# Performance work log

Hardware: AMD Instinct MI355X
Metric: run time of the kernel (lower is better)

Reference implementation:

```python
import jax, jax.numpy as jnp
import numpy as np

DIM = 512
HEADS = 8
HEAD_DIM = DIM // HEADS
SCALE = HEAD_DIM ** -0.5
CPB_HIDDEN = 512
N_CLASSES = 2
LN_EPS = 1e-5


def _layernorm(x, g, b):
    m = jnp.mean(x, axis=-1, keepdims=True)
    v = jnp.var(x, axis=-1, keepdims=True)
    return (x - m) / jnp.sqrt(v + LN_EPS) * g + b


def _coord_attention(x, coords, cpb_w1, cpb_b1, cpb_w2, cpb_b2, qkv_w, qkv_b, proj_w, proj_b):
    B, N, C = x.shape
    qkv = (x @ qkv_w + qkv_b).reshape(B, N, 3, HEADS, HEAD_DIM)
    q, k, v = jnp.moveaxis(qkv, 2, 0)  # each (B, N, H, hd)
    attn = jnp.einsum('bnhd,bmhd->bhnm', q * SCALE, k)  # (B, H, N, N)
    rel = coords[:, :, None, :] - coords[:, None, :, :]  # (B, N, N, 2)
    rel = rel / (jnp.linalg.norm(rel, axis=-1, keepdims=True) + 1e-6)
    bias = jax.nn.relu(rel @ cpb_w1 + cpb_b1) @ cpb_w2 + cpb_b2  # (B, N, N, H)
    attn = jax.nn.softmax(attn + jnp.transpose(bias, (0, 3, 1, 2)), axis=-1)
    out = jnp.einsum('bhnm,bmhd->bnhd', attn, v).reshape(B, N, C)
    return out @ proj_w + proj_b


def setup_inputs() -> dict:
    key = jax.random.key(0)
    ks = iter(jax.random.split(key, 32))
    d = {}
    d['h'] = jax.random.normal(next(ks), (1, 400, 1024), dtype=jnp.float32)
    d['coords'] = jax.random.uniform(next(ks), (1, 400, 2), dtype=jnp.float32) * 1000.0
    def lin(kw, kb, fan_in, fan_out):
        w = jax.random.normal(kw, (fan_in, fan_out), dtype=jnp.float32) / np.sqrt(fan_in)
        b = jax.random.normal(kb, (fan_out,), dtype=jnp.float32) * 0.01
        return w, b
    d['fc1_w'], d['fc1_b'] = lin(next(ks), next(ks), 1024, DIM)
    d['cls_token'] = jax.random.normal(next(ks), (1, 1, DIM), dtype=jnp.float32)
    for p in ('l1', 'l2'):
        d[p + '_norm_g'] = jnp.ones((DIM,), jnp.float32)
        d[p + '_norm_b'] = jnp.zeros((DIM,), jnp.float32)
        d[p + '_cpb_w1'], d[p + '_cpb_b1'] = lin(next(ks), next(ks), 2, CPB_HIDDEN)
        d[p + '_cpb_w2'], d[p + '_cpb_b2'] = lin(next(ks), next(ks), CPB_HIDDEN, HEADS)
        d[p + '_qkv_w'], d[p + '_qkv_b'] = lin(next(ks), next(ks), DIM, 3 * DIM)
        d[p + '_proj_w'], d[p + '_proj_b'] = lin(next(ks), next(ks), DIM, DIM)
    d['norm_g'] = jnp.ones((DIM,), jnp.float32)
    d['norm_b'] = jnp.zeros((DIM,), jnp.float32)
    d['fc2_w'], d['fc2_b'] = lin(next(ks), next(ks), DIM, N_CLASSES)
    return d


def reference(h, coords, fc1_w, fc1_b, cls_token,
              l1_norm_g, l1_norm_b, l1_cpb_w1, l1_cpb_b1, l1_cpb_w2, l1_cpb_b2,
              l1_qkv_w, l1_qkv_b, l1_proj_w, l1_proj_b,
              l2_norm_g, l2_norm_b, l2_cpb_w1, l2_cpb_b1, l2_cpb_w2, l2_cpb_b2,
              l2_qkv_w, l2_qkv_b, l2_proj_w, l2_proj_b,
              norm_g, norm_b, fc2_w, fc2_b):
    B, Np, _ = h.shape
    h = jax.nn.relu(h @ fc1_w + fc1_b)  # (B, N, 512)
    side = int(np.ceil(np.sqrt(Np)))
    add = side * side - Np  # pad bag to a perfect square (wrap-around copy)
    h = jnp.concatenate([h, h[:, :add, :]], axis=1)
    coords = jnp.concatenate([coords, coords[:, :add, :]], axis=1)
    cls = jnp.broadcast_to(cls_token, (B, 1, DIM))
    h = jnp.concatenate([cls, h], axis=1)
    coords = jnp.concatenate([jnp.zeros((B, 1, 2), h.dtype), coords], axis=1)
    h = h + _coord_attention(_layernorm(h, l1_norm_g, l1_norm_b), coords,
                             l1_cpb_w1, l1_cpb_b1, l1_cpb_w2, l1_cpb_b2,
                             l1_qkv_w, l1_qkv_b, l1_proj_w, l1_proj_b)
    h = h + _coord_attention(_layernorm(h, l2_norm_g, l2_norm_b), coords,
                             l2_cpb_w1, l2_cpb_b1, l2_cpb_w2, l2_cpb_b2,
                             l2_qkv_w, l2_qkv_b, l2_proj_w, l2_proj_b)
    h = _layernorm(h, norm_g, norm_b)[:, 0]  # CLS token
    return h @ fc2_w + fc2_b  # (B, n_classes)
```

## Files before the change

### kernel.cpp

```cpp
#include <hip/hip_runtime.h>
#include <math.h>

#define NP 401
#define DIM 512
#define LN_EPS 1e-5f
#define ATT_SCALE 0.125f
#define CPB_M 4096
#define TSTRIDE (CPB_M + 64)
#define PVS (401L * 512)

template<bool TB, typename LA, typename LB>
__device__ __forceinline__ void gemm64(
    int kBeg, int kEnd, int tid,
    float (*as)[68], float (*bs)[68], float (&acc)[4][4],
    LA&& loadA, LB&& loadB)
{
    float aR[4], bR[4];
    loadA(kBeg, aR);
    loadB(kBeg, bR);
    for (int k0 = kBeg; k0 < kEnd; k0 += 16) {
        const int arow = tid >> 2, aq = tid & 3;
        as[aq * 4 + 0][arow] = aR[0];
        as[aq * 4 + 1][arow] = aR[1];
        as[aq * 4 + 2][arow] = aR[2];
        as[aq * 4 + 3][arow] = aR[3];
        if (!TB) {
            *(float4*)&bs[tid >> 4][(tid & 15) * 4] =
                make_float4(bR[0], bR[1], bR[2], bR[3]);
        } else {
            bs[aq * 4 + 0][arow] = bR[0];
            bs[aq * 4 + 1][arow] = bR[1];
            bs[aq * 4 + 2][arow] = bR[2];
            bs[aq * 4 + 3][arow] = bR[3];
        }
        __syncthreads();
        float nA[4] = {0.f,0.f,0.f,0.f}, nB[4] = {0.f,0.f,0.f,0.f};
        if (k0 + 16 < kEnd) { loadA(k0 + 16, nA); loadB(k0 + 16, nB); }
        const int tx = tid & 15, ty = tid >> 4;
        #pragma unroll
        for (int kk = 0; kk < 16; ++kk) {
            float4 a4 = *(const float4*)&as[kk][ty * 4];
            float4 b4 = *(const float4*)&bs[kk][tx * 4];
            float av[4] = {a4.x, a4.y, a4.z, a4.w};
            float bv[4] = {b4.x, b4.y, b4.z, b4.w};
            #pragma unroll
            for (int r = 0; r < 4; ++r)
                #pragma unroll
                for (int c = 0; c < 4; ++c)
                    acc[r][c] = fmaf(av[r], bv[c], acc[r][c]);
        }
        __syncthreads();
        #pragma unroll
        for (int j = 0; j < 4; ++j) { aR[j] = nA[j]; bR[j] = nB[j]; }
    }
}

__global__ __launch_bounds__(256) void gemm_bias_kernel(
    const float* __restrict__ A,
    const float* __restrict__ B, int ldb,
    const float* __restrict__ bias,
    float* __restrict__ C, int ldc)
{
    __shared__ float as[16][68], bs[16][68];
    const int tid = threadIdx.x;
    const int m0 = blockIdx.x * 64, n0 = blockIdx.y * 64;
    float acc[4][4] = {};

    auto loadA = [&](int k0, float r[4]) {
        int gm = m0 + (tid >> 2);
        if (gm > 400) { r[0]=r[1]=r[2]=r[3]=0.f; return; }
        int gk = k0 + (tid & 3) * 4;
        float4 v = *(const float4*)(A + (long)gm * 512 + gk);
        r[0]=v.x; r[1]=v.y; r[2]=v.z; r[3]=v.w;
    };
    auto loadB = [&](int k0, float r[4]) {
        int gk = k0 + (tid >> 4);
        int gn = n0 + (tid & 15) * 4;
        float4 v = *(const float4*)(B + (long)gk * ldb + gn);
        r[0]=v.x; r[1]=v.y; r[2]=v.z; r[3]=v.w;
    };
    gemm64<false>(0, 512, tid, as, bs, acc, loadA, loadB);

    const int tx = tid & 15, ty = tid >> 4;
    const float4 bv = *(const float4*)(bias + n0 + tx * 4);
    #pragma unroll
    for (int r = 0; r < 4; ++r) {
        int m = m0 + ty * 4 + r;
        if (m > 400) continue;
        *(float4*)&C[(long)m * ldc + n0 + tx * 4] =
            make_float4(acc[r][0] + bv.x, acc[r][1] + bv.y,
                        acc[r][2] + bv.z, acc[r][3] + bv.w);
    }
}

__global__ __launch_bounds__(256) void flash_kernel(
    const float* __restrict__ qkv,
    const int* __restrict__ pm, const float* __restrict__ pf,
    const float* __restrict__ T,
    float* __restrict__ PO,
    float* __restrict__ Pml)
{
    __shared__ float as[16][68], bs[16][68];
    __shared__ float pT[64][68];
    __shared__ float vs[64][68];
    const int tid = threadIdx.x;
    const int m0 = blockIdx.x * 64, nb = blockIdx.y, h = blockIdx.z;
    const int n0 = nb * 64;
    float acc[4][4] = {};

    float vreg[4][4];
    {
        int key = n0 + (tid >> 2);
        int d0 = (tid & 3) * 16;
        if (key <= 400) {
            const float* p = qkv + (long)key * 1536 + 1024 + h * 64 + d0;
            #pragma unroll
            for (int i = 0; i < 4; ++i) {
                float4 v = *(const float4*)(p + i * 4);
                vreg[i][0] = v.x; vreg[i][1] = v.y;
                vreg[i][2] = v.z; vreg[i][3] = v.w;
            }
        } else {
            #pragma unroll
            for (int i = 0; i < 4; ++i)
                vreg[i][0] = vreg[i][1] = vreg[i][2] = vreg[i][3] = 0.f;
        }
    }

    auto loadQ = [&](int k0, float r[4]) {
        int gm = m0 + (tid >> 2);
        if (gm > 400) { r[0]=r[1]=r[2]=r[3]=0.f; return; }
        int gk = k0 + (tid & 3) * 4;
        float4 v = *(const float4*)(qkv + (long)gm * 1536 + h * 64 + gk);
        r[0]=v.x; r[1]=v.y; r[2]=v.z; r[3]=v.w;
    };
    auto loadK = [&](int k0, float r[4]) {
        int gn = n0 + (tid >> 2);
        if (gn > 400) { r[0]=r[1]=r[2]=r[3]=0.f; return; }
        int gk = k0 + (tid & 3) * 4;
        float4 v = *(const float4*)(qkv + (long)gn * 1536 + 512 + h * 64 + gk);
        r[0]=v.x; r[1]=v.y; r[2]=v.z; r[3]=v.w;
    };
    gemm64<true>(0, 64, tid, as, bs, acc, loadQ, loadK);

    {
        int key = tid >> 2, d0 = (tid & 3) * 16;
        #pragma unroll
        for (int i = 0; i < 4; ++i)
            *(float4*)&vs[key][d0 + i * 4] =
                make_float4(vreg[i][0], vreg[i][1], vreg[i][2], vreg[i][3]);
    }

    const int tx = tid & 15, ty = tid >> 4;
    const float* Tt = T + (long)h * TSTRIDE;
    float p[4][4];
    #pragma unroll
    for (int r = 0; r < 4; ++r) {
        int i = m0 + ty * 4 + r;
        float sv[4];
        #pragma unroll
        for (int c = 0; c < 4; ++c) {
            int j = n0 + tx * 4 + c;
            if (i <= 400 && j <= 400) {
                int id = i * 416 + j;
                int mm = pm[id];
                float fr = pf[id];
                float t0 = Tt[mm], t1 = Tt[mm + 1];
                sv[c] = fmaf(acc[r][c], ATT_SCALE, fmaf(fr, t1 - t0, t0));
            } else {
                sv[c] = -INFINITY;
            }
        }
        float cmax = fmaxf(fmaxf(sv[0], sv[1]), fmaxf(sv[2], sv[3]));
        cmax = fmaxf(cmax, __shfl_xor(cmax, 1));
        cmax = fmaxf(cmax, __shfl_xor(cmax, 2));
        cmax = fmaxf(cmax, __shfl_xor(cmax, 4));
        cmax = fmaxf(cmax, __shfl_xor(cmax, 8));
        const bool rowok = (i <= 400);
        #pragma unroll
        for (int c = 0; c < 4; ++c)
            p[r][c] = rowok ? __expf(sv[c] - cmax) : 0.f;
        float cs = p[r][0] + p[r][1] + p[r][2] + p[r][3];
        cs += __shfl_xor(cs, 1);
        cs += __shfl_xor(cs, 2);
        cs += __shfl_xor(cs, 4);
        cs += __shfl_xor(cs, 8);
        if (tx == 0 && rowok) {
            long o = ((long)(h * 401 + i) * 7 + nb) * 2;
            Pml[o] = cmax;
            Pml[o + 1] = cs;
        }
    }
    #pragma unroll
    for (int c = 0; c < 4; ++c)
        *(float4*)&pT[tx * 4 + c][ty * 4] =
            make_float4(p[0][c], p[1][c], p[2][c], p[3][c]);
    __syncthreads();

    float o[4][4] = {};
    #pragma unroll 16
    for (int kk = 0; kk < 64; ++kk) {
        float4 a4 = *(const float4*)&pT[kk][ty * 4];
        float4 b4 = *(const float4*)&vs[kk][tx * 4];
        float av[4] = {a4.x, a4.y, a4.z, a4.w};
        float bv[4] = {b4.x, b4.y, b4.z, b4.w};
        #pragma unroll
        for (int r = 0; r < 4; ++r)
            #pragma unroll
            for (int c = 0; c < 4; ++c)
                o[r][c] = fmaf(av[r], bv[c], o[r][c]);
    }

    float* C = PO + (long)nb * PVS;
    #pragma unroll
    for (int r = 0; r < 4; ++r) {
        int m = m0 + ty * 4 + r;
        if (m > 400) continue;
        *(float4*)&C[(long)m * 512 + h * 64 + tx * 4] =
            make_float4(o[r][0], o[r][1], o[r][2], o[r][3]);
    }
}

__global__ __launch_bounds__(256) void proj_kernel(
    const float* __restrict__ PO, const float* __restrict__ Pml,
    const float* __restrict__ projw, float* __restrict__ Pp)
{
    __shared__ float as[16][68], bs[16][68];
    __shared__ float wls[64][8];
    const int tid = threadIdx.x;
    const int m0 = blockIdx.x * 64, n0 = blockIdx.y * 64, sk = blockIdx.z;
    const int kBeg = sk * 64, kEnd = kBeg + 64;
    float acc[4][4] = {};

    if (tid < 64) {
        int row = m0 + tid;
        if (row <= 400) {
            const float* q = Pml + ((long)(sk * 401 + row) * 7) * 2;
            float M = -INFINITY;
            #pragma unroll
            for (int c = 0; c < 7; ++c) M = fmaxf(M, q[c * 2]);
            float D = 0.f;
            #pragma unroll
            for (int c = 0; c < 7; ++c) D += q[c * 2 + 1] * __expf(q[c * 2] - M);
            float iD = 1.f / D;
            #pragma unroll
            for (int c = 0; c < 7; ++c) wls[tid][c] = __expf(q[c * 2] - M) * iD;
        } else {
            #pragma unroll
            for (int c = 0; c < 7; ++c) wls[tid][c] = 0.f;
        }
    }
    __syncthreads();

    auto loadA = [&](int k0, float r4[4]) {
        r4[0] = r4[1] = r4[2] = r4[3] = 0.f;
        int lm = tid >> 2, gm = m0 + lm;
        if (gm > 400) return;
        int gk = k0 + (tid & 3) * 4;
        #pragma unroll
        for (int s = 0; s < 7; ++s) {
            float4 v = *(const float4*)(PO + (long)s * PVS + (long)gm * 512 + gk);
            float w = wls[lm][s];
            r4[0] = fmaf(w, v.x, r4[0]);
            r4[1] = fmaf(w, v.y, r4[1]);
            r4[2] = fmaf(w, v.z, r4[2]);
            r4[3] = fmaf(w, v.w, r4[3]);
        }
    };
    auto loadB = [&](int k0, float r[4]) {
        int gk = k0 + (tid >> 4);
        int gn = n0 + (tid & 15) * 4;
        float4 v = *(const float4*)(projw + (long)gk * 512 + gn);
        r[0]=v.x; r[1]=v.y; r[2]=v.z; r[3]=v.w;
    };
    gemm64<false>(kBeg, kEnd, tid, as, bs, acc, loadA, loadB);

    float* C = Pp + (long)sk * PVS;
    const int tx = tid & 15, ty = tid >> 4;
    #pragma unroll
    for (int r = 0; r < 4; ++r) {
        int m = m0 + ty * 4 + r;
        if (m > 400) continue;
        *(float4*)&C[(long)m * 512 + n0 + tx * 4] =
            make_float4(acc[r][0], acc[r][1], acc[r][2], acc[r][3]);
    }
}

__global__ __launch_bounds__(256) void rowfuse_kernel(
    const float* __restrict__ P, long slice, int skN, int rowOff,
    const float* __restrict__ bias, int doRelu,
    const float* __restrict__ resid, const float* __restrict__ cls,
    float* __restrict__ h0,
    const float* __restrict__ g, const float* __restrict__ b,
    float* __restrict__ xln)
{
    const int r = blockIdx.x, t = threadIdx.x;
    float v0, v1;
    if (cls && r == 0) {
        v0 = cls[t]; v1 = cls[t + 256];
    } else {
        const float* p = P + (long)(r - rowOff) * DIM;
        v0 = bias[t]; v1 = bias[t + 256];
        for (int k = 0; k < skN; ++k) {
            v0 += p[(long)k * slice + t];
            v1 += p[(long)k * slice + t + 256];
        }
        if (resid) {
            v0 += resid[(long)r * DIM + t];
            v1 += resid[(long)r * DIM + t + 256];
        }
        if (doRelu) { v0 = fmaxf(v0, 0.f); v1 = fmaxf(v1, 0.f); }
    }
    h0[(long)r * DIM + t] = v0;
    h0[(long)r * DIM + t + 256] = v1;

    float s = v0 + v1, sq = v0 * v0 + v1 * v1;
    #pragma unroll
    for (int off = 32; off > 0; off >>= 1) {
        s += __shfl_down(s, off);
        sq += __shfl_down(sq, off);
    }
    __shared__ float ps[4], pq[4];
    int w = t >> 6, lane = t & 63;
    if (lane == 0) { ps[w] = s; pq[w] = sq; }
    __syncthreads();
    float Sm = ps[0] + ps[1] + ps[2] + ps[3];
    float Q = pq[0] + pq[1] + pq[2] + pq[3];
    float mean = Sm * (1.f / DIM);
    float var = Q * (1.f / DIM) - mean * mean;
    float inv = rsqrtf(var + LN_EPS);
    xln[(long)r * DIM + t]       = (v0 - mean) * inv * g[t] + b[t];
    xln[(long)r * DIM + t + 256] = (v1 - mean) * inv * g[t + 256] + b[t + 256];
}

__global__ __launch_bounds__(256) void cls_decode_kernel(
    const float* __restrict__ xln, const float* __restrict__ qkvw,
    const float* __restrict__ kv, const float* __restrict__ qkvb,
    const int* __restrict__ pm, const float* __restrict__ pf,
    const float* __restrict__ T,
    float* __restrict__ cms, float* __restrict__ cpv,
    unsigned* __restrict__ cnt)
{
    const int h = blockIdx.x, c = blockIdx.y, tid = threadIdx.x;
    const int kBeg = c * 64;
    __shared__ float q0[64], scraw[64], p[64], red[4][64], rr[2];

    if (h == 0 && c == 0 && tid == 0) *cnt = 0u;

    {
        int d = tid & 63, w4 = tid >> 6;
        const float* col = qkvw + h * 64 + d;
        float acc = 0.f;
        for (int k = w4 * 128; k < w4 * 128 + 128; ++k)
            acc = fmaf(xln[k], col[(long)k * 1536], acc);
        red[w4][d] = acc;
    }
    __syncthreads();
    if (tid < 64)
        q0[tid] = red[0][tid] + red[1][tid] + red[2][tid] + red[3][tid]
                  + qkvb[h * 64 + tid];
    __syncthreads();

    {
        int k = tid >> 2, q = tid & 3;
        int j = kBeg + k;
        float dot = 0.f;
        if (j < NP) {
            long base = (long)j * 1024 + h * 64 + q * 16;
            #pragma unroll
            for (int d = 0; d < 16; d += 4) {
                float4 x0 = *(const float4*)(kv + base + d);
                float4 qq = *(const float4*)(q0 + q * 16 + d);
                dot = fmaf(qq.x, x0.x, dot);
                dot = fmaf(qq.y, x0.y, dot);
                dot = fmaf(qq.z, x0.z, dot);
                dot = fmaf(qq.w, x0.w, dot);
            }
        }
        dot += __shfl_down(dot, 2);
        dot += __shfl_down(dot, 1);
        if (q == 0) scraw[k] = dot;
    }
    __syncthreads();

    if (tid < 64) {
        int j = kBeg + tid;
        float s;
        if (j < NP) {
            int mm = pm[j];
            float fr = pf[j];
            const float* Tt = T + (long)h * TSTRIDE;
            float t0 = Tt[mm], t1 = Tt[mm + 1];
            s = fmaf(scraw[tid], ATT_SCALE, fmaf(fr, t1 - t0, t0));
        } else {
            s = -INFINITY;
        }
        float m = s;
        #pragma unroll
        for (int off = 32; off > 0; off >>= 1)
            m = fmaxf(m, __shfl_xor(m, off));
        float e = (j < NP) ? __expf(s - m) : 0.f;
        float sum = e;
        #pragma unroll
        for (int off = 32; off > 0; off >>= 1)
            sum += __shfl_xor(sum, off);
        p[tid] = e;
        if (tid == 0) { rr[0] = m; rr[1] = sum; }
    }
    __syncthreads();

    {
        int w = tid >> 6, d = tid & 63;
        float acc = 0.f;
        for (int k = w; k < 64; k += 4) {
            int j = kBeg + k;
            if (j >= NP) break;
            long o = (long)j * 1024 + 512 + h * 64 + d;
            acc = fmaf(p[k], kv[o], acc);
        }
        red[w][d] = acc;
    }
    __syncthreads();
    if (tid < 64) {
        cpv[((long)h * 7 + c) * 64 + tid] =
            red[0][tid] + red[1][tid] + red[2][tid] + red[3][tid];
        if (tid == 0) {
            cms[(h * 7 + c) * 2 + 0] = rr[0];
            cms[(h * 7 + c) * 2 + 1] = rr[1];
        }
    }
}

__global__ __launch_bounds__(256) void cls_proj_kernel(
    const float* __restrict__ cms, const float* __restrict__ cpv,
    const float* __restrict__ projw, const float* __restrict__ projb,
    float* __restrict__ proj0,
    const float* __restrict__ h0,
    const float* __restrict__ g, const float* __restrict__ b,
    const float* __restrict__ fc2w, const float* __restrict__ fc2b,
    float* __restrict__ out, unsigned* __restrict__ cnt)
{
    __shared__ float av[512], red[4][64];
    __shared__ int isLast;
    const int bk = blockIdx.x, tid = threadIdx.x;
    for (int d = tid; d < 512; d += 256) {
        int h = d >> 6, dd = d & 63;
        float M = -INFINITY;
        #pragma unroll
        for (int c = 0; c < 7; ++c)
            M = fmaxf(M, cms[(h * 7 + c) * 2]);
        float Sx = 0.f, acc = 0.f;
        #pragma unroll
        for (int c = 0; c < 7; ++c) {
            float e = __expf(cms[(h * 7 + c) * 2] - M);
            Sx += cms[(h * 7 + c) * 2 + 1] * e;
            acc += cpv[((long)h * 7 + c) * 64 + dd] * e;
        }
        av[d] = acc / Sx;
    }
    __syncthreads();
    int gg = tid >> 6, n = bk * 64 + (tid & 63);
    float acc = 0.f;
    for (int k = gg * 128; k < gg * 128 + 128; ++k)
        acc = fmaf(av[k], projw[(long)k * 512 + n], acc);
    red[gg][tid & 63] = acc;
    __syncthreads();
    if (tid < 64)
        proj0[bk * 64 + tid] = red[0][tid] + red[1][tid] + red[2][tid]
                               + red[3][tid] + projb[bk * 64 + tid];

    __threadfence();
    if (tid == 0) isLast = (atomicAdd(cnt, 1u) == 7u);
    __syncthreads();
    if (!isLast) return;
    __threadfence();

    const int t = tid;
    float v0 = h0[t] + proj0[t];
    float v1 = h0[t + 256] + proj0[t + 256];
    float s = v0 + v1, sq = v0 * v0 + v1 * v1;
    #pragma unroll
    for (int off = 32; off > 0; off >>= 1) {
        s += __shfl_down(s, off);
        sq += __shfl_down(sq, off);
    }
    __shared__ float ps[4], pq[4], pc0[4], pc1[4];
    int w = t >> 6, lane = t & 63;
    if (lane == 0) { ps[w] = s; pq[w] = sq; }
    __syncthreads();
    float Sm = ps[0] + ps[1] + ps[2] + ps[3];
    float Q = pq[0] + pq[1] + pq[2] + pq[3];
    float mean = Sm * (1.f / DIM);
    float var = Q * (1.f / DIM) - mean * mean;
    float inv = rsqrtf(var + LN_EPS);
    float n0 = (v0 - mean) * inv * g[t] + b[t];
    float n1 = (v1 - mean) * inv * g[t + 256] + b[t + 256];
    float c0 = n0 * fc2w[t * 2]     + n1 * fc2w[(t + 256) * 2];
    float c1 = n0 * fc2w[t * 2 + 1] + n1 * fc2w[(t + 256) * 2 + 1];
    #pragma unroll
    for (int off = 32; off > 0; off >>= 1) {
        c0 += __shfl_down(c0, off);
        c1 += __shfl_down(c1, off);
    }
    if (lane == 0) { pc0[w] = c0; pc1[w] = c1; }
    __syncthreads();
    if (t == 0) {
        out[0] = pc0[0] + pc0[1] + pc0[2] + pc0[3] + fc2b[0];
        out[1] = pc1[0] + pc1[1] + pc1[2] + pc1[3] + fc2b[1];
    }
}

__global__ __launch_bounds__(256) void mega_kernel(
    const float* __restrict__ hin, const float* __restrict__ fc1_w,
    const float* __restrict__ w1_0, const float* __restrict__ b1_0,
    const float* __restrict__ w2_0, const float* __restrict__ b2_0,
    const float* __restrict__ w1_1, const float* __restrict__ b1_1,
    const float* __restrict__ w2_1, const float* __restrict__ b2_1,
    const float* __restrict__ coords,
    float* __restrict__ Pp, float* __restrict__ T,
    int* __restrict__ pm, float* __restrict__ pf)
{
    __shared__ float smem[2176];
    float (*as)[68] = (float(*)[68])smem;
    float (*bs)[68] = (float(*)[68])(smem + 1088);
    float (*red)[64][8] = (float(*)[64][8])smem;
    const int bid = blockIdx.x, tid = threadIdx.x;

    if (bid < 224) {
        int sk = bid / 56, rem = bid % 56;
        int m0 = (rem % 7) * 64, n0 = (rem / 7) * 64;
        int kBeg = sk * 256, kEnd = kBeg + 256;
        float acc[4][4] = {};
        auto loadA = [&](int k0, float r[4]) {
            r[0]=r[1]=r[2]=r[3]=0.f;
            int gm = m0 + (tid >> 2);
            if (gm >= 400) return;
            int gk = k0 + (tid & 3) * 4;
            float4 v = *(const float4*)(hin + (long)gm * 1024 + gk);
            r[0]=v.x; r[1]=v.y; r[2]=v.z; r[3]=v.w;
        };
        auto loadB = [&](int k0, float r[4]) {
            int gk = k0 + (tid >> 4);
            int gn = n0 + (tid & 15) * 4;
            float4 v = *(const float4*)(fc1_w + (long)gk * 512 + gn);
            r[0]=v.x; r[1]=v.y; r[2]=v.z; r[3]=v.w;
        };
        gemm64<false>(kBeg, kEnd, tid, as, bs, acc, loadA, loadB);
        float* C = Pp + (long)sk * PVS;
        const int tx = tid & 15, ty = tid >> 4;
        #pragma unroll
        for (int r = 0; r < 4; ++r) {
            int m = m0 + ty * 4 + r;
            if (m >= 400) continue;
            *(float4*)&C[(long)m * 512 + n0 + tx * 4] =
                make_float4(acc[r][0], acc[r][1], acc[r][2], acc[r][3]);
        }
    } else if (bid < 354) {
        int tb = bid - 224;
        int z = tb / 65, ab = tb % 65;
        const float* w1 = z ? w1_1 : w1_0;
        const float* b1 = z ? b1_1 : b1_0;
        const float* w2 = z ? w2_1 : w2_0;
        const float* b2 = z ? b2_1 : b2_0;
        const int lane = tid & 63, wv = tid >> 6;
        float ca = 0.f, sa = 0.f;
        if (ab != 64) {
            float th = fmaf((float)(ab * 64 + lane),
                            (float)(2.0 * M_PI / CPB_M), -(float)M_PI);
            sincosf(th, &sa, &ca);
        } else if (lane == 0) {
            sincosf((float)M_PI, &sa, &ca);
        }
        float a8[8] = {};
        const int kbeg = wv * 128;
        #pragma unroll 4
        for (int k = kbeg; k < kbeg + 128; ++k) {
            float hk = fmaxf(fmaf(ca, w1[k],
                                  fmaf(sa, w1[512 + k], b1[k])), 0.f);
            #pragma unroll
            for (int h2 = 0; h2 < 8; ++h2)
                a8[h2] = fmaf(hk, w2[k * 8 + h2], a8[h2]);
        }
        #pragma unroll
        for (int h2 = 0; h2 < 8; ++h2) red[wv][lane][h2] = a8[h2];
        __syncthreads();
        if (tid < 64) {
            int aidx = ab * 64 + tid;
            if (aidx <= CPB_M + 1) {
                #pragma unroll
                for (int h2 = 0; h2 < 8; ++h2)
                    T[(long)(z * 8 + h2) * TSTRIDE + aidx] =
                        red[0][tid][h2] + red[1][tid][h2] +
                        red[2][tid][h2] + red[3][tid][h2] + b2[h2];
            }
        }
    } else {
        int p = (bid - 354) * 256 + tid;
        if (p < NP * NP) {
            int i = p / NP, j = p - i * NP;
            float xi = (i == 0) ? 0.f : coords[(i - 1) * 2];
            float yi = (i == 0) ? 0.f : coords[(i - 1) * 2 + 1];
            float xj = (j == 0) ? 0.f : coords[(j - 1) * 2];
            float yj = (j == 0) ? 0.f : coords[(j - 1) * 2 + 1];
            float rx = xi - xj, ry = yi - yj;
            int mm; float fr;
            if (rx == 0.f && ry == 0.f) {
                mm = CPB_M + 1; fr = 0.f;
            } else {
                float x = (atan2f(ry, rx) + 3.14159265358979f)
                          * (float)(CPB_M / (2.0 * M_PI));
                int mi = (int)x;
                fr = x - (float)mi;
                mm = (mi >= CPB_M) ? mi - CPB_M : mi;
            }
            pm[i * 416 + j] = mm;
            pf[i * 416 + j] = fr;
        }
    }
}

extern "C" void kernel_launch(void* const* d_in, const int* in_sizes, int n_in,
                              void* d_out, int out_size, void* d_ws, size_t ws_size,
                              hipStream_t stream)
{
    const float* coords = (const float*)d_in[1];
    float* ws = (float*)d_ws;
    float* h0   = ws;                    ws += 401L * 512;
    float* xln  = ws;                    ws += 401L * 512;
    float* PO   = ws;                    ws += 7L * PVS;
    float* T    = ws;                    ws += 16L * TSTRIDE;
    int*   pm   = (int*)ws;              ws += 401L * 416;
    float* pf   = ws;                    ws += 401L * 416;
    float* kv   = ws;                    ws += 401L * 1024;
    float* qkv  = ws;                    ws += 401L * 1536;
    float* Pp   = ws;                    ws += 8L * PVS;
    float* proj0 = ws;                   ws += 512;
    float* cms  = ws;                    ws += 8L * 7 * 2;
    float* cpv  = ws;                    ws += 8L * 7 * 64;
    float* Pml  = ws;                    ws += 8L * 401 * 7 * 2;
    unsigned* cnt = (unsigned*)ws;       ws += 16;

    mega_kernel<<<983, 256, 0, stream>>>(
        (const float*)d_in[0], (const float*)d_in[2],
        (const float*)d_in[7],  (const float*)d_in[8],
        (const float*)d_in[9],  (const float*)d_in[10],
        (const float*)d_in[17], (const float*)d_in[18],
        (const float*)d_in[19], (const float*)d_in[20],
        coords, Pp, T, pm, pf);

    rowfuse_kernel<<<401, 256, 0, stream>>>(
        Pp, PVS, 4, 1, (const float*)d_in[3], 1, nullptr,
        (const float*)d_in[4], h0,
        (const float*)d_in[5], (const float*)d_in[6], xln);

    gemm_bias_kernel<<<dim3(7, 24), 256, 0, stream>>>(
        xln, (const float*)d_in[11], 1536, (const float*)d_in[12],
        qkv, 1536);
    flash_kernel<<<dim3(7, 7, 8), 256, 0, stream>>>(
        qkv, pm, pf, T, PO, Pml);
    proj_kernel<<<dim3(7, 8, 8), 256, 0, stream>>>(
        PO, Pml, (const float*)d_in[13], Pp);
    rowfuse_kernel<<<401, 256, 0, stream>>>(
        Pp, PVS, 8, 0, (const float*)d_in[14], 0, h0, nullptr, h0,
        (const float*)d_in[15], (const float*)d_in[16], xln);

    gemm_bias_kernel<<<dim3(7, 16), 256, 0, stream>>>(
        xln, (const float*)d_in[21] + 512, 1536, (const float*)d_in[22] + 512,
        kv, 1024);
    cls_decode_kernel<<<dim3(8, 7), 256, 0, stream>>>(
        xln, (const float*)d_in[21], kv, (const float*)d_in[22],
        pm, pf, T + 8L * TSTRIDE, cms, cpv, cnt);
    cls_proj_kernel<<<8, 256, 0, stream>>>(
        cms, cpv, (const float*)d_in[23], (const float*)d_in[24], proj0,
        h0, (const float*)d_in[25], (const float*)d_in[26],
        (const float*)d_in[27], (const float*)d_in[28], (float*)d_out, cnt);
}
```

Before: 242.7 us.

## Split-K 64x256 GEMM tiles for QKV/KV and fc1, reduce partials in consumers

Replaces the 64x64 QKV and KV bias GEMMs with a 64x256-tile split-K GEMM using eight K-slices. It writes partial sums to a workspace, and the flash and cls_decode kernels sum the eight partials plus bias when they load Q/K/V. fc1 in the mega kernel moves to the same 64x256 tile with sixteen K-slices, summed in rowfuse. The aim is more parallel blocks and more register reuse per block. The cost is extra partial-sum memory traffic and repeated 8-way reductions inside the attention loads, since each K/V row is re-read by many query blocks.

```diff
diff --git a/kernel.cpp b/kernel.cpp
--- a/kernel.cpp
+++ b/kernel.cpp
@@ -7,6 +7,8 @@
 #define ATT_SCALE 0.125f
 #define CPB_M 4096
 #define TSTRIDE (CPB_M + 64)
+#define PQS (401L * 1536)
+#define PKS (401L * 1024)
 #define PVS (401L * 512)
 
 template<bool TB, typename LA, typename LB>
@@ -55,46 +57,108 @@
     }
 }
 
-__global__ __launch_bounds__(256) void gemm_bias_kernel(
-    const float* __restrict__ A,
+template<typename LA, typename LB>
+__device__ __forceinline__ void gemm256(
+    int kBeg, int kEnd, int tid,
+    float (*as)[68], float (*bs)[260], float (&acc)[4][4][4],
+    LA&& loadA, LB&& loadB)
+{
+    float aR[4], bR[4][4];
+    loadA(kBeg, aR);
+    loadB(kBeg, bR);
+    for (int k0 = kBeg; k0 < kEnd; k0 += 16) {
+        const int arow = tid >> 2, aq = tid & 3;
+        as[aq * 4 + 0][arow] = aR[0];
+        as[aq * 4 + 1][arow] = aR[1];
+        as[aq * 4 + 2][arow] = aR[2];
+        as[aq * 4 + 3][arow] = aR[3];
+        {
+            const int brow = tid >> 4, bcol = (tid & 15) * 4;
+            #pragma unroll
+            for (int j = 0; j < 4; ++j)
+                *(float4*)&bs[brow][bcol + 64 * j] =
+                    make_float4(bR[j][0], bR[j][1], bR[j][2], bR[j][3]);
+        }
+        __syncthreads();
+        float nA[4] = {0.f,0.f,0.f,0.f};
+        float nB[4][4] = {};
+        if (k0 + 16 < kEnd) { loadA(k0 + 16, nA); loadB(k0 + 16, nB); }
+        const int tx = tid & 15, ty = tid >> 4;
+        #pragma unroll
+        for (int kk = 0; kk < 16; ++kk) {
+            float4 a4 = *(const float4*)&as[kk][ty * 4];
+            float av[4] = {a4.x, a4.y, a4.z, a4.w};
+            #pragma unroll
+            for (int j = 0; j < 4; ++j) {
+                float4 b4 = *(const float4*)&bs[kk][tx * 4 + 64 * j];
+                float bv[4] = {b4.x, b4.y, b4.z, b4.w};
+                #pragma unroll
+                for (int r = 0; r < 4; ++r)
+                    #pragma unroll
+                    for (int c = 0; c < 4; ++c)
+                        acc[r][j][c] = fmaf(av[r], bv[c], acc[r][j][c]);
+            }
+        }
+        __syncthreads();
+        #pragma unroll
+        for (int i = 0; i < 4; ++i) aR[i] = nA[i];
+        #pragma unroll
+        for (int j = 0; j < 4; ++j)
+            #pragma unroll
+            for (int i = 0; i < 4; ++i) bR[j][i] = nB[j][i];
+    }
+}
+
+__global__ __launch_bounds__(256) void gemm_split256_kernel(
+    const float* __restrict__ A, int lda,
     const float* __restrict__ B, int ldb,
-    const float* __restrict__ bias,
-    float* __restrict__ C, int ldc)
-{
-    __shared__ float as[16][68], bs[16][68];
+    float* __restrict__ P, int ldc, long slice,
+    int M, int K, int skN)
+{
+    __shared__ float as[16][68], bs[16][260];
     const int tid = threadIdx.x;
-    const int m0 = blockIdx.x * 64, n0 = blockIdx.y * 64;
-    float acc[4][4] = {};
+    const int m0 = blockIdx.x * 64, n0 = blockIdx.y * 256;
+    const int sk = blockIdx.z;
+    const int KS = K / skN;
+    const int kBeg = sk * KS, kEnd = kBeg + KS;
+    float acc[4][4][4] = {};
 
     auto loadA = [&](int k0, float r[4]) {
+        r[0] = r[1] = r[2] = r[3] = 0.f;
         int gm = m0 + (tid >> 2);
-        if (gm > 400) { r[0]=r[1]=r[2]=r[3]=0.f; return; }
+        if (gm >= M) return;
         int gk = k0 + (tid & 3) * 4;
-        float4 v = *(const float4*)(A + (long)gm * 512 + gk);
+        float4 v = *(const float4*)(A + (long)gm * lda + gk);
         r[0]=v.x; r[1]=v.y; r[2]=v.z; r[3]=v.w;
     };
-    auto loadB = [&](int k0, float r[4]) {
+    auto loadB = [&](int k0, float r[4][4]) {
         int gk = k0 + (tid >> 4);
-        int gn = n0 + (tid & 15) * 4;
-        float4 v = *(const float4*)(B + (long)gk * ldb + gn);
-        r[0]=v.x; r[1]=v.y; r[2]=v.z; r[3]=v.w;
+        const float* p = B + (long)gk * ldb + n0 + (tid & 15) * 4;
+        #pragma unroll
+        for (int j = 0; j < 4; ++j) {
+            float4 v = *(const float4*)(p + 64 * j);
+            r[j][0]=v.x; r[j][1]=v.y; r[j][2]=v.z; r[j][3]=v.w;
+        }
     };
-    gemm64<false>(0, 512, tid, as, bs, acc, loadA, loadB);
-
+    gemm256(kBeg, kEnd, tid, as, bs, acc, loadA, loadB);
+
+    float* C = P + (long)sk * slice;
     const int tx = tid & 15, ty = tid >> 4;
-    const float4 bv = *(const float4*)(bias + n0 + tx * 4);
     #pragma unroll
     for (int r = 0; r < 4; ++r) {
         int m = m0 + ty * 4 + r;
-        if (m > 400) continue;
-        *(float4*)&C[(long)m * ldc + n0 + tx * 4] =
-            make_float4(acc[r][0] + bv.x, acc[r][1] + bv.y,
-                        acc[r][2] + bv.z, acc[r][3] + bv.w);
+        if (m >= M) continue;
+        #pragma unroll
+        for (int j = 0; j < 4; ++j)
+            *(float4*)&C[(long)m * ldc + n0 + tx * 4 + 64 * j] =
+                make_float4(acc[r][j][0], acc[r][j][1],
+                            acc[r][j][2], acc[r][j][3]);
     }
 }
 
 __global__ __launch_bounds__(256) void flash_kernel(
-    const float* __restrict__ qkv,
+    const float* __restrict__ Pq,
+    const float* __restrict__ qkvb,
     const int* __restrict__ pm, const float* __restrict__ pf,
     const float* __restrict__ T,
     float* __restrict__ PO,
@@ -113,12 +177,18 @@
         int key = n0 + (tid >> 2);
         int d0 = (tid & 3) * 16;
         if (key <= 400) {
-            const float* p = qkv + (long)key * 1536 + 1024 + h * 64 + d0;
+            long base = (long)key * 1536 + 1024 + h * 64 + d0;
             #pragma unroll
             for (int i = 0; i < 4; ++i) {
-                float4 v = *(const float4*)(p + i * 4);
-                vreg[i][0] = v.x; vreg[i][1] = v.y;
-                vreg[i][2] = v.z; vreg[i][3] = v.w;
+                float4 bb = *(const float4*)(qkvb + 1024 + h * 64 + d0 + i * 4);
+                float r0 = bb.x, r1 = bb.y, r2 = bb.z, r3 = bb.w;
+                #pragma unroll
+                for (int s = 0; s < 8; ++s) {
+                    float4 v = *(const float4*)(Pq + (long)s * PQS + base + i * 4);
+                    r0 += v.x; r1 += v.y; r2 += v.z; r3 += v.w;
+                }
+                vreg[i][0] = r0; vreg[i][1] = r1;
+                vreg[i][2] = r2; vreg[i][3] = r3;
             }
         } else {
             #pragma unroll
@@ -131,15 +201,27 @@
         int gm = m0 + (tid >> 2);
         if (gm > 400) { r[0]=r[1]=r[2]=r[3]=0.f; return; }
         int gk = k0 + (tid & 3) * 4;
-        float4 v = *(const float4*)(qkv + (long)gm * 1536 + h * 64 + gk);
-        r[0]=v.x; r[1]=v.y; r[2]=v.z; r[3]=v.w;
+        long base = (long)gm * 1536 + h * 64 + gk;
+        float4 bb = *(const float4*)(qkvb + h * 64 + gk);
+        r[0] = bb.x; r[1] = bb.y; r[2] = bb.z; r[3] = bb.w;
+        #pragma unroll
+        for (int s = 0; s < 8; ++s) {
+            float4 v = *(const float4*)(Pq + (long)s * PQS + base);
+            r[0] += v.x; r[1] += v.y; r[2] += v.z; r[3] += v.w;
+        }
     };
     auto loadK = [&](int k0, float r[4]) {
         int gn = n0 + (tid >> 2);
         if (gn > 400) { r[0]=r[1]=r[2]=r[3]=0.f; return; }
         int gk = k0 + (tid & 3) * 4;
-        float4 v = *(const float4*)(qkv + (long)gn * 1536 + 512 + h * 64 + gk);
-        r[0]=v.x; r[1]=v.y; r[2]=v.z; r[3]=v.w;
+        long base = (long)gn * 1536 + 512 + h * 64 + gk;
+        float4 bb = *(const float4*)(qkvb + 512 + h * 64 + gk);
+        r[0] = bb.x; r[1] = bb.y; r[2] = bb.z; r[3] = bb.w;
+        #pragma unroll
+        for (int s = 0; s < 8; ++s) {
+            float4 v = *(const float4*)(Pq + (long)s * PQS + base);
+            r[0] += v.x; r[1] += v.y; r[2] += v.z; r[3] += v.w;
+        }
     };
     gemm64<true>(0, 64, tid, as, bs, acc, loadQ, loadK);
 
@@ -335,7 +417,7 @@
 
 __global__ __launch_bounds__(256) void cls_decode_kernel(
     const float* __restrict__ xln, const float* __restrict__ qkvw,
-    const float* __restrict__ kv, const float* __restrict__ qkvb,
+    const float* __restrict__ Pkv, const float* __restrict__ qkvb,
     const int* __restrict__ pm, const float* __restrict__ pf,
     const float* __restrict__ T,
     float* __restrict__ cms, float* __restrict__ cpv,
@@ -369,12 +451,17 @@
             long base = (long)j * 1024 + h * 64 + q * 16;
             #pragma unroll
             for (int d = 0; d < 16; d += 4) {
-                float4 x0 = *(const float4*)(kv + base + d);
+                float4 x = *(const float4*)(qkvb + 512 + h * 64 + q * 16 + d);
+                #pragma unroll
+                for (int s = 0; s < 8; ++s) {
+                    float4 v = *(const float4*)(Pkv + (long)s * PKS + base + d);
+                    x.x += v.x; x.y += v.y; x.z += v.z; x.w += v.w;
+                }
                 float4 qq = *(const float4*)(q0 + q * 16 + d);
-                dot = fmaf(qq.x, x0.x, dot);
-                dot = fmaf(qq.y, x0.y, dot);
-                dot = fmaf(qq.z, x0.z, dot);
-                dot = fmaf(qq.w, x0.w, dot);
+                dot = fmaf(qq.x, x.x, dot);
+                dot = fmaf(qq.y, x.y, dot);
+                dot = fmaf(qq.z, x.z, dot);
+                dot = fmaf(qq.w, x.w, dot);
             }
         }
         dot += __shfl_down(dot, 2);
@@ -411,12 +498,16 @@
 
     {
         int w = tid >> 6, d = tid & 63;
+        float vb = qkvb[1024 + h * 64 + d];
         float acc = 0.f;
         for (int k = w; k < 64; k += 4) {
             int j = kBeg + k;
             if (j >= NP) break;
             long o = (long)j * 1024 + 512 + h * 64 + d;
-            acc = fmaf(p[k], kv[o], acc);
+            float v = vb;
+            #pragma unroll
+            for (int s = 0; s < 8; ++s) v += Pkv[(long)s * PKS + o];
+            acc = fmaf(p[k], v, acc);
         }
         red[w][d] = acc;
     }
@@ -520,17 +611,17 @@
     float* __restrict__ Pp, float* __restrict__ T,
     int* __restrict__ pm, float* __restrict__ pf)
 {
-    __shared__ float smem[2176];
-    float (*as)[68] = (float(*)[68])smem;
-    float (*bs)[68] = (float(*)[68])(smem + 1088);
+    __shared__ float smem[5248];
+    float (*as)[68]  = (float(*)[68])smem;
+    float (*bs)[260] = (float(*)[260])(smem + 1088);
     float (*red)[64][8] = (float(*)[64][8])smem;
     const int bid = blockIdx.x, tid = threadIdx.x;
 
     if (bid < 224) {
-        int sk = bid / 56, rem = bid % 56;
-        int m0 = (rem % 7) * 64, n0 = (rem / 7) * 64;
-        int kBeg = sk * 256, kEnd = kBeg + 256;
-        float acc[4][4] = {};
+        int sk = bid / 14, rem = bid % 14;
+        int m0 = (rem % 7) * 64, n0 = (rem / 7) * 256;
+        int kBeg = sk * 64, kEnd = kBeg + 64;
+        float acc[4][4][4] = {};
         auto loadA = [&](int k0, float r[4]) {
             r[0]=r[1]=r[2]=r[3]=0.f;
             int gm = m0 + (tid >> 2);
@@ -539,21 +630,27 @@
             float4 v = *(const float4*)(hin + (long)gm * 1024 + gk);
             r[0]=v.x; r[1]=v.y; r[2]=v.z; r[3]=v.w;
         };
-        auto loadB = [&](int k0, float r[4]) {
+        auto loadB = [&](int k0, float r[4][4]) {
             int gk = k0 + (tid >> 4);
-            int gn = n0 + (tid & 15) * 4;
-            float4 v = *(const float4*)(fc1_w + (long)gk * 512 + gn);
-            r[0]=v.x; r[1]=v.y; r[2]=v.z; r[3]=v.w;
+            const float* p = fc1_w + (long)gk * 512 + n0 + (tid & 15) * 4;
+            #pragma unroll
+            for (int j = 0; j < 4; ++j) {
+                float4 v = *(const float4*)(p + 64 * j);
+                r[j][0]=v.x; r[j][1]=v.y; r[j][2]=v.z; r[j][3]=v.w;
+            }
         };
-        gemm64<false>(kBeg, kEnd, tid, as, bs, acc, loadA, loadB);
+        gemm256(kBeg, kEnd, tid, as, bs, acc, loadA, loadB);
         float* C = Pp + (long)sk * PVS;
         const int tx = tid & 15, ty = tid >> 4;
         #pragma unroll
         for (int r = 0; r < 4; ++r) {
             int m = m0 + ty * 4 + r;
             if (m >= 400) continue;
-            *(float4*)&C[(long)m * 512 + n0 + tx * 4] =
-                make_float4(acc[r][0], acc[r][1], acc[r][2], acc[r][3]);
+            #pragma unroll
+            for (int j = 0; j < 4; ++j)
+                *(float4*)&C[(long)m * 512 + n0 + tx * 4 + 64 * j] =
+                    make_float4(acc[r][j][0], acc[r][j][1],
+                                acc[r][j][2], acc[r][j][3]);
         }
     } else if (bid < 354) {
         int tb = bid - 224;
@@ -631,9 +728,8 @@
     float* T    = ws;                    ws += 16L * TSTRIDE;
     int*   pm   = (int*)ws;              ws += 401L * 416;
     float* pf   = ws;                    ws += 401L * 416;
-    float* kv   = ws;                    ws += 401L * 1024;
-    float* qkv  = ws;                    ws += 401L * 1536;
-    float* Pp   = ws;                    ws += 8L * PVS;
+    float* Pq   = ws;                    ws += 8L * PQS;
+    float* Pp   = ws;                    ws += 16L * PVS;
     float* proj0 = ws;                   ws += 512;
     float* cms  = ws;                    ws += 8L * 7 * 2;
     float* cpv  = ws;                    ws += 8L * 7 * 64;
@@ -649,26 +745,26 @@
         coords, Pp, T, pm, pf);
 
     rowfuse_kernel<<<401, 256, 0, stream>>>(
-        Pp, PVS, 4, 1, (const float*)d_in[3], 1, nullptr,
+        Pp, PVS, 16, 1, (const float*)d_in[3], 1, nullptr,
         (const float*)d_in[4], h0,
         (const float*)d_in[5], (const float*)d_in[6], xln);
 
-    gemm_bias_kernel<<<dim3(7, 24), 256, 0, stream>>>(
-        xln, (const float*)d_in[11], 1536, (const float*)d_in[12],
-        qkv, 1536);
+    gemm_split256_kernel<<<dim3(7, 6, 8), 256, 0, stream>>>(
+        xln, 512, (const float*)d_in[11], 1536, Pq, 1536, PQS,
+        401, 512, 8);
     flash_kernel<<<dim3(7, 7, 8), 256, 0, stream>>>(
-        qkv, pm, pf, T, PO, Pml);
+        Pq, (const float*)d_in[12], pm, pf, T, PO, Pml);
     proj_kernel<<<dim3(7, 8, 8), 256, 0, stream>>>(
         PO, Pml, (const float*)d_in[13], Pp);
     rowfuse_kernel<<<401, 256, 0, stream>>>(
         Pp, PVS, 8, 0, (const float*)d_in[14], 0, h0, nullptr, h0,
         (const float*)d_in[15], (const float*)d_in[16], xln);
 
-    gemm_bias_kernel<<<dim3(7, 16), 256, 0, stream>>>(
-        xln, (const float*)d_in[21] + 512, 1536, (const float*)d_in[22] + 512,
-        kv, 1024);
+    gemm_split256_kernel<<<dim3(7, 4, 8), 256, 0, stream>>>(
+        xln, 512, (const float*)d_in[21] + 512, 1536, Pq, 1024, PKS,
+        401, 512, 8);
     cls_decode_kernel<<<dim3(8, 7), 256, 0, stream>>>(
-        xln, (const float*)d_in[21], kv, (const float*)d_in[22],
+        xln, (const float*)d_in[21], Pq, (const float*)d_in[22],
         pm, pf, T + 8L * TSTRIDE, cms, cpv, cnt);
     cls_proj_kernel<<<8, 256, 0, stream>>>(
         cms, cpv, (const float*)d_in[23], (const float*)d_in[24], proj0,
```

After: 266.2 us. 1.1x slower.
